# Performance work log

Measured on AMD Instinct MI355X. Metric: run time of the kernel, lower is better.

Reference implementation:

```python
import jax, jax.numpy as jnp
import numpy as np

B, L, D, H = 2, 2048, 1024, 16


def setup_inputs() -> dict:
    key = jax.random.key(0)
    ks = jax.random.split(key, 6)
    return {
        "x": jax.random.normal(ks[0], (B, L, D), dtype=jnp.float32),
        "w_qkv": jax.random.normal(ks[1], (3 * D, D), dtype=jnp.float32) * (D ** -0.5),
        "b_qkv": jax.random.normal(ks[2], (3 * D,), dtype=jnp.float32) * 0.02,
        "w_out": jax.random.normal(ks[3], (D, D), dtype=jnp.float32) * (D ** -0.5),
        "b_out": jax.random.normal(ks[4], (D,), dtype=jnp.float32) * 0.02,
        "lam": jnp.float32(0.5),
        "heads": H,
    }


def reference(x, w_qkv, b_qkv, w_out, b_out, lam, heads):
    b, l, d = x.shape
    dh = d // heads
    scale = d ** -0.5  # NOTE: module scales by d_model**-0.5, not head_dim**-0.5

    qkv = x @ w_qkv.T + b_qkv                      # [B, L, 3D]
    qkv = qkv.reshape(b, l, 3, heads, dh)
    qkv = jnp.transpose(qkv, (2, 0, 3, 1, 4))      # [3, B, H, L, dh]
    q, k, v = qkv[0], qkv[1], qkv[2]

    k_prev = jnp.roll(k, shift=1, axis=2)          # roll along sequence dim

    s_cur = jnp.einsum("bhqd,bhkd->bhqk", q, k) * scale
    s_prev = jnp.einsum("bhqd,bhkd->bhqk", q, k_prev) * scale

    a1 = jax.nn.softmax(s_cur, axis=-1)
    a2 = jax.nn.softmax(s_prev, axis=-1)
    diff = lam * (a1 - a2)                         # dropout = identity (eval)

    o = jnp.einsum("bhqk,bhkd->bhqd", diff, v)     # [B, H, L, dh]
    o = jnp.transpose(o, (0, 2, 1, 3)).reshape(b, l, d)
    return o @ w_out.T + b_out
```

## Files before the change

kernel.cpp:

```cpp
#include <hip/hip_runtime.h>
#include <hip/hip_bf16.h>
#include <stdint.h>


typedef __attribute__((ext_vector_type(8))) short s16x8;
typedef __attribute__((ext_vector_type(4))) short s16x4;
typedef __attribute__((ext_vector_type(4))) float f32x4;
typedef __attribute__((ext_vector_type(4))) unsigned int u32x4;

__device__ __forceinline__ float bf2f(unsigned short u) {
    union { unsigned int i; float f; } x; x.i = ((unsigned int)u) << 16; return x.f;
}
__device__ __forceinline__ unsigned short f2bf(float f) {
    union { float f; unsigned int i; } x; x.f = f;
    unsigned int r = x.i + 0x7FFFu + ((x.i >> 16) & 1u);
    return (unsigned short)(r >> 16);
}

__device__ __forceinline__ unsigned int cvtpk(float lo, float hi) {
    unsigned int r;
    asm("v_cvt_pk_bf16_f32 %0, %1, %2" : "=v"(r) : "v"(lo), "v"(hi));
    return r;
}

__device__ __forceinline__ void gload16(const void* g, void* l) {
    auto gp = reinterpret_cast<const __attribute__((address_space(1))) unsigned int*>(
        reinterpret_cast<uintptr_t>(g));
    auto lp = reinterpret_cast<__attribute__((address_space(3))) unsigned int*>(
        reinterpret_cast<uintptr_t>(l));
    __builtin_amdgcn_global_load_lds(gp, lp, 16, 0, 0);
}

__global__ __launch_bounds__(256) void cvt_all(
    const float* __restrict__ x, const float* __restrict__ wq,
    const float* __restrict__ wo,
    unsigned short* __restrict__ xb, unsigned short* __restrict__ wqb,
    unsigned short* __restrict__ wob)
{
    int i4 = blockIdx.x * 256 + threadIdx.x;
    const float* src; unsigned short* dst; int off;
    if (i4 < 1048576)            { src = x;  dst = xb;  off = i4; }
    else if (i4 < 1048576 + 786432) { src = wq; dst = wqb; off = i4 - 1048576; }
    else                         { src = wo; dst = wob; off = i4 - 1835008; }
    float4 v = ((const float4*)src)[off];
    ushort4 u;
    u.x = f2bf(v.x); u.y = f2bf(v.y); u.z = f2bf(v.z); u.w = f2bf(v.w);
    ((ushort4*)dst)[off] = u;
}

__global__ __launch_bounds__(256) void vd_transpose(
    const unsigned short* __restrict__ qkvb, unsigned short* __restrict__ vdt)
{
    __shared__ unsigned short T[64][72];
    const int tid = threadIdx.x;
    const int j0 = blockIdx.x * 64;
    const int bh = blockIdx.y, b = bh >> 4, h = bh & 15;
    const unsigned short* vb = qkvb + (size_t)b * 2048 * 3072 + 2048 + h * 64;

    int r = tid >> 2, cq = tid & 3;
    int rp = (r & 35) | ((r & 12) << 1) | ((r & 16) >> 2);
    int j = j0 + r, jn = (j + 1) & 2047;
    const unsigned short* p0 = vb + (size_t)j  * 3072 + cq * 16;
    const unsigned short* p1 = vb + (size_t)jn * 3072 + cq * 16;
    s16x8 a0 = *(const s16x8*)p0, a1 = *(const s16x8*)(p0 + 8);
    s16x8 b0 = *(const s16x8*)p1, b1 = *(const s16x8*)(p1 + 8);
#pragma unroll
    for (int u = 0; u < 8; ++u)
        T[cq * 16 + u][rp] = f2bf(bf2f((unsigned short)a0[u]) - bf2f((unsigned short)b0[u]));
#pragma unroll
    for (int u = 0; u < 8; ++u)
        T[cq * 16 + 8 + u][rp] = f2bf(bf2f((unsigned short)a1[u]) - bf2f((unsigned short)b1[u]));
    __syncthreads();

    int row = tid >> 2, sc = tid & 3;
    s16x8 o0 = *(const s16x8*)&T[row][sc * 16];
    s16x8 o1 = *(const s16x8*)&T[row][sc * 16 + 8];
    unsigned short* dst = vdt + ((size_t)bh * 64 + row) * 2048 + j0 + sc * 16;
    *(s16x8*)dst = o0;
    *(s16x8*)(dst + 8) = o1;
}

template <int OUT_BF16, int BN>
__global__ __launch_bounds__(256) void gemm_nt_mfma(
    const unsigned short* __restrict__ A,
    const unsigned short* __restrict__ Bm,
    const float* __restrict__ bias,
    void* __restrict__ C,
    int M, int N, int K, int nscale, float smul)
{
    constexpr int NT = BN / 32;
    __shared__ unsigned short As[2][128][32];
    __shared__ unsigned short Bs[2][BN][32];

    const int tid = threadIdx.x;
    const int wave = tid >> 6, lane = tid & 63;
    const int quad = lane >> 4, ln = lane & 15;
    const int wm = (wave >> 1) * 64, wn = (wave & 1) * (NT * 16);
    const int m0 = blockIdx.y * 128, n0 = blockIdx.x * BN;
    const int rA = wave * 16 + (lane >> 2);
    const int gsl = lane & 3;

    f32x4 acc[4][NT];
#pragma unroll
    for (int mt = 0; mt < 4; ++mt)
#pragma unroll
        for (int nt = 0; nt < NT; ++nt) acc[mt][nt] = f32x4{0.f, 0.f, 0.f, 0.f};

    auto stage = [&](int p, int k0) {
#pragma unroll
        for (int q = 0; q < 2; ++q) {
            int row = q * 64 + rA;
            int kg = gsl ^ ((row >> 1) & 3);
            gload16(A + (size_t)(m0 + row) * K + k0 + kg * 8,
                    &As[p][q * 64 + wave * 16][0]);
            if (q * 64 < BN)
                gload16(Bm + (size_t)(n0 + row) * K + k0 + kg * 8,
                        &Bs[p][q * 64 + wave * 16][0]);
        }
    };

    stage(0, 0);
    __syncthreads();
    int p = 0;
    for (int k0 = 0; k0 < K; k0 += 32) {
        if (k0 + 32 < K) stage(p ^ 1, k0 + 32);
        s16x8 af[4], bfr[NT];
#pragma unroll
        for (int mt = 0; mt < 4; ++mt) {
            int rr = wm + mt * 16 + ln;
            af[mt] = *(const s16x8*)&As[p][rr][((quad ^ ((rr >> 1) & 3)) & 3) * 8];
        }
#pragma unroll
        for (int nt = 0; nt < NT; ++nt) {
            int rr = wn + nt * 16 + ln;
            bfr[nt] = *(const s16x8*)&Bs[p][rr][((quad ^ ((rr >> 1) & 3)) & 3) * 8];
        }
#pragma unroll
        for (int mt = 0; mt < 4; ++mt)
#pragma unroll
            for (int nt = 0; nt < NT; ++nt)
                acc[mt][nt] = __builtin_amdgcn_mfma_f32_16x16x32_bf16(
                    af[mt], bfr[nt], acc[mt][nt], 0, 0, 0);
        __syncthreads();
        p ^= 1;
    }

    float bb[NT];
#pragma unroll
    for (int nt = 0; nt < NT; ++nt) bb[nt] = bias[n0 + wn + nt * 16 + ln];
#pragma unroll
    for (int mt = 0; mt < 4; ++mt)
#pragma unroll
        for (int nt = 0; nt < NT; ++nt) {
            int col = n0 + wn + nt * 16 + ln;
            float sc = (col < nscale) ? smul : 1.f;
#pragma unroll
            for (int rg = 0; rg < 4; ++rg) {
                int row = m0 + wm + mt * 16 + quad * 4 + rg;
                float v = (acc[mt][nt][rg] + bb[nt]) * sc;
                if (OUT_BF16)
                    ((unsigned short*)C)[(size_t)row * N + col] = f2bf(v);
                else
                    ((float*)C)[(size_t)row * N + col] = v;
            }
        }
}

__global__ __launch_bounds__(512) void diff_attn_v10(
    const unsigned short* __restrict__ qkv,
    const unsigned short* __restrict__ vdt,
    const float* __restrict__ lam_p,
    unsigned short* __restrict__ o_ws)
{
    constexpr int L = 2048, TD = 3072;

    __shared__ __align__(16) unsigned char smem[65536];
    auto Ks = reinterpret_cast<unsigned short(*)[64][64]>(smem);
    auto Vs = reinterpret_cast<unsigned short(*)[64][64]>(smem + 32768);
    auto Red = reinterpret_cast<f32x4(*)[2][4][64]>(smem);
    auto Lred = reinterpret_cast<float(*)[2][64]>(smem + 32768);

    const int tid = threadIdx.x;
    const int wave = tid >> 6, lane = tid & 63;
    const int qw = wave & 3, jw = wave >> 2;
    const int quad = lane >> 4, ln = lane & 15;
    const int bh = blockIdx.y, b = bh >> 4, h = bh & 15;
    const int q0 = blockIdx.x * 128;
    const size_t seqbase = (size_t)b * L;
    const unsigned short* base = qkv + seqbase * TD + h * 64;
    const unsigned short* kb = base + 1024;
    const unsigned short* vbase = vdt + (size_t)bh * 64 * 2048;

    const int lsl = lane >> 3;
    const int cgl = (lane & 7) ^ lsl;

    const float lam = lam_p[0];
    asm volatile("" :: "v"(lam));

    s16x8 qf[2][2];
#pragma unroll
    for (int s = 0; s < 2; ++s) {
        const unsigned short* qrow =
            base + (size_t)(q0 + qw * 32 + s * 16 + ln) * TD;
        qf[s][0] = *(const s16x8*)(qrow + quad * 8);
        qf[s][1] = *(const s16x8*)(qrow + 32 + quad * 8);
    }

    const unsigned short* kstage = kb + (size_t)(wave * 8 + lsl) * TD + cgl * 8;
    const unsigned short* vstage = vbase + (size_t)(wave * 8 + lsl) * 2048 + cgl * 8;

    f32x4 Ot[2][4];
    f32x4 lacc[2];
#pragma unroll
    for (int s = 0; s < 2; ++s) {
        lacc[s] = f32x4{0.f, 0.f, 0.f, 0.f};
#pragma unroll
        for (int mt = 0; mt < 4; ++mt) Ot[s][mt] = f32x4{0.f, 0.f, 0.f, 0.f};
    }

    const s16x8 ones8 = {(short)0x3F80, (short)0x3F80, (short)0x3F80, (short)0x3F80,
                         (short)0x3F80, (short)0x3F80, (short)0x3F80, (short)0x3F80};
    const int kx0 = (quad ^ (ln & 7)) << 3;
    const int kx1 = ((quad + 4) ^ (ln & 7)) << 3;
    const int vx  = (((jw * 4 + quad) ^ (ln & 7))) << 3;

    auto body = [&](auto cc, auto ccs, int j0s) {
        constexpr int c  = decltype(cc)::value;
        constexpr int cs = decltype(ccs)::value;

        gload16(kstage + (size_t)j0s * TD, &Ks[cs][wave * 8][0]);
        gload16(vstage + j0s,              &Vs[cs][wave * 8][0]);

        f32x4 ST[2][2];
        __builtin_amdgcn_s_setprio(1);
#pragma unroll
        for (int t = 0; t < 2; ++t) {
            const int t2 = jw * 2 + t;
            s16x8 k0 = *(const s16x8*)&Ks[c][t2 * 16 + ln][kx0];
            s16x8 k1 = *(const s16x8*)&Ks[c][t2 * 16 + ln][kx1];
#pragma unroll
            for (int s = 0; s < 2; ++s) {
                f32x4 z = f32x4{0.f, 0.f, 0.f, 0.f};
                z = __builtin_amdgcn_mfma_f32_16x16x32_bf16(k0, qf[s][0], z, 0, 0, 0);
                z = __builtin_amdgcn_mfma_f32_16x16x32_bf16(k1, qf[s][1], z, 0, 0, 0);
                ST[s][t] = z;
            }
        }
        __builtin_amdgcn_s_setprio(0);

        s16x8 pf8[2];
#pragma unroll
        for (int s = 0; s < 2; ++s) {
            unsigned int w[4];
#pragma unroll
            for (int t = 0; t < 2; ++t) {
                float e0 = __builtin_amdgcn_exp2f(ST[s][t][0]);
                float e1 = __builtin_amdgcn_exp2f(ST[s][t][1]);
                float e2 = __builtin_amdgcn_exp2f(ST[s][t][2]);
                float e3 = __builtin_amdgcn_exp2f(ST[s][t][3]);
                w[t * 2]     = cvtpk(e0, e1);
                w[t * 2 + 1] = cvtpk(e2, e3);
            }
            pf8[s] = __builtin_bit_cast(s16x8, (u32x4){w[0], w[1], w[2], w[3]});
        }

        __builtin_amdgcn_s_setprio(1);
#pragma unroll
        for (int s = 0; s < 2; ++s)
            lacc[s] = __builtin_amdgcn_mfma_f32_16x16x32_bf16(
                ones8, pf8[s], lacc[s], 0, 0, 0);
#pragma unroll
        for (int mt = 0; mt < 4; ++mt) {
            s16x8 vf = *(const s16x8*)&Vs[c][mt * 16 + ln][vx];
#pragma unroll
            for (int s = 0; s < 2; ++s)
                Ot[s][mt] = __builtin_amdgcn_mfma_f32_16x16x32_bf16(
                    vf, pf8[s], Ot[s][mt], 0, 0, 0);
        }
        __builtin_amdgcn_s_setprio(0);

        asm volatile("s_waitcnt vmcnt(2)" ::: "memory");
        __builtin_amdgcn_s_barrier();
        asm volatile("" ::: "memory");
    };

    gload16(kstage, &Ks[0][wave * 8][0]);
    gload16(vstage, &Vs[0][wave * 8][0]);
    gload16(kstage + (size_t)64 * TD, &Ks[1][wave * 8][0]);
    gload16(vstage + 64,              &Vs[1][wave * 8][0]);
    asm volatile("s_waitcnt vmcnt(2)" ::: "memory");
    __builtin_amdgcn_s_barrier();
    asm volatile("" ::: "memory");

    using I0 = std::integral_constant<int, 0>;
    using I1 = std::integral_constant<int, 1>;
    using I2 = std::integral_constant<int, 2>;
    using I3 = std::integral_constant<int, 3>;
    for (int it = 0; it < 8; ++it) {
        const int kt4 = it * 4;
        body(I0{}, I2{}, ((kt4 + 2) & 31) * 64);
        body(I1{}, I3{}, ((kt4 + 3) & 31) * 64);
        body(I2{}, I0{}, ((kt4 + 4) & 31) * 64);
        body(I3{}, I1{}, ((kt4 + 5) & 31) * 64);
    }

    __syncthreads();

    if (jw == 1) {
#pragma unroll
        for (int s = 0; s < 2; ++s) {
            Lred[qw][s][lane] = lacc[s][0];
#pragma unroll
            for (int mt = 0; mt < 4; ++mt) Red[qw][s][mt][lane] = Ot[s][mt];
        }
    }
    __syncthreads();
    if (jw == 0) {
#pragma unroll
        for (int s = 0; s < 2; ++s) {
            float lsum = lacc[s][0] + Lred[qw][s][lane];
            float inv = lam / lsum;
            int row = q0 + qw * 32 + s * 16 + ln;
            unsigned short* orow = o_ws + (seqbase + row) * 1024 + h * 64 + quad * 4;
#pragma unroll
            for (int mt = 0; mt < 4; ++mt) {
                f32x4 r = Red[qw][s][mt][lane];
                ushort4 u;
                u.x = f2bf((Ot[s][mt][0] + r[0]) * inv);
                u.y = f2bf((Ot[s][mt][1] + r[1]) * inv);
                u.z = f2bf((Ot[s][mt][2] + r[2]) * inv);
                u.w = f2bf((Ot[s][mt][3] + r[3]) * inv);
                *(ushort4*)(orow + mt * 16) = u;
            }
        }
    }
}

extern "C" void kernel_launch(void* const* d_in, const int* in_sizes, int n_in,
                              void* d_out, int out_size, void* d_ws, size_t ws_size,
                              hipStream_t stream) {
    const float* x     = (const float*)d_in[0];
    const float* w_qkv = (const float*)d_in[1];
    const float* b_qkv = (const float*)d_in[2];
    const float* w_out = (const float*)d_in[3];
    const float* b_out = (const float*)d_in[4];
    const float* lam   = (const float*)d_in[5];
    float* out = (float*)d_out;

    unsigned short* xb   = (unsigned short*)d_ws;
    unsigned short* wqb  = xb   + (size_t)4096 * 1024;
    unsigned short* wob  = wqb  + (size_t)3072 * 1024;
    unsigned short* qkvb = wob  + (size_t)1024 * 1024;
    unsigned short* ob   = qkvb + (size_t)4096 * 3072;
    unsigned short* vdt  = ob   + (size_t)4096 * 1024;

    cvt_all<<<8192, 256, 0, stream>>>(x, w_qkv, w_out, xb, wqb, wob);

    gemm_nt_mfma<1, 128><<<dim3(24, 32), 256, 0, stream>>>(
        xb, wqb, b_qkv, qkvb, 4096, 3072, 1024, 1024, 0.045084222f);

    vd_transpose<<<dim3(32, 32), 256, 0, stream>>>(qkvb, vdt);

    diff_attn_v10<<<dim3(16, 32), 512, 0, stream>>>(qkvb, vdt, lam, ob);

    gemm_nt_mfma<0, 64><<<dim3(16, 32), 256, 0, stream>>>(
        ob, wob, b_out, out, 4096, 1024, 1024, 0, 1.f);
}
```

Measured before the change: 184.5 us.

## Fuse fp32-to-bf16 conversion into GEMM tile staging, drop separate convert kernel

Removes the standalone conversion kernel that turned x, w_qkv and w_out into bf16 copies. The GEMMs now load fp32 tiles into registers, pack them to bf16 and write them into LDS after the MFMA step, which keeps prefetch overlap. This saves a launch and the bf16 write and re-read round trip. In exchange the GEMMs read twice as many bytes from global memory, and the weights are re-converted by every block that touches them instead of once.

```diff
diff --git a/kernel.cpp b/kernel.cpp
--- a/kernel.cpp
+++ b/kernel.cpp
@@ -29,23 +29,6 @@
     auto lp = reinterpret_cast<__attribute__((address_space(3))) unsigned int*>(
         reinterpret_cast<uintptr_t>(l));
     __builtin_amdgcn_global_load_lds(gp, lp, 16, 0, 0);
-}
-
-__global__ __launch_bounds__(256) void cvt_all(
-    const float* __restrict__ x, const float* __restrict__ wq,
-    const float* __restrict__ wo,
-    unsigned short* __restrict__ xb, unsigned short* __restrict__ wqb,
-    unsigned short* __restrict__ wob)
-{
-    int i4 = blockIdx.x * 256 + threadIdx.x;
-    const float* src; unsigned short* dst; int off;
-    if (i4 < 1048576)            { src = x;  dst = xb;  off = i4; }
-    else if (i4 < 1048576 + 786432) { src = wq; dst = wqb; off = i4 - 1048576; }
-    else                         { src = wo; dst = wob; off = i4 - 1835008; }
-    float4 v = ((const float4*)src)[off];
-    ushort4 u;
-    u.x = f2bf(v.x); u.y = f2bf(v.y); u.z = f2bf(v.z); u.w = f2bf(v.w);
-    ((ushort4*)dst)[off] = u;
 }
 
 __global__ __launch_bounds__(256) void vd_transpose(
@@ -80,10 +63,10 @@
     *(s16x8*)(dst + 8) = o1;
 }
 
-template <int OUT_BF16, int BN>
+template <int OUT_BF16, int BN, int CVT_A, int CVT_B>
 __global__ __launch_bounds__(256) void gemm_nt_mfma(
-    const unsigned short* __restrict__ A,
-    const unsigned short* __restrict__ Bm,
+    const void* __restrict__ Ap,
+    const void* __restrict__ Bp,
     const float* __restrict__ bias,
     void* __restrict__ C,
     int M, int N, int K, int nscale, float smul)
@@ -106,24 +89,61 @@
 #pragma unroll
         for (int nt = 0; nt < NT; ++nt) acc[mt][nt] = f32x4{0.f, 0.f, 0.f, 0.f};
 
-    auto stage = [&](int p, int k0) {
+    float4 ra[2][2], rb[2][2];
+
+    auto ld8f = [&](const float* src, int row, int k0, float4* d) {
+        int kg = gsl ^ ((row >> 1) & 3);
+        const float* p = src + (size_t)row * K + k0 + kg * 8;
+        d[0] = *(const float4*)p;
+        d[1] = *(const float4*)(p + 4);
+    };
+
+    auto stage_loads = [&](int pn, int k0) {
 #pragma unroll
         for (int q = 0; q < 2; ++q) {
             int row = q * 64 + rA;
-            int kg = gsl ^ ((row >> 1) & 3);
-            gload16(A + (size_t)(m0 + row) * K + k0 + kg * 8,
-                    &As[p][q * 64 + wave * 16][0]);
-            if (q * 64 < BN)
-                gload16(Bm + (size_t)(n0 + row) * K + k0 + kg * 8,
-                        &Bs[p][q * 64 + wave * 16][0]);
-        }
-    };
-
-    stage(0, 0);
+            if (CVT_A) {
+                ld8f((const float*)Ap, m0 + row, k0, ra[q]);
+            } else {
+                int kg = gsl ^ ((row >> 1) & 3);
+                gload16((const unsigned short*)Ap + (size_t)(m0 + row) * K + k0 + kg * 8,
+                        &As[pn][q * 64 + wave * 16][0]);
+            }
+            if (q * 64 < BN) {
+                if (CVT_B) {
+                    ld8f((const float*)Bp, n0 + row, k0, rb[q]);
+                } else {
+                    int kg = gsl ^ ((row >> 1) & 3);
+                    gload16((const unsigned short*)Bp + (size_t)(n0 + row) * K + k0 + kg * 8,
+                            &Bs[pn][q * 64 + wave * 16][0]);
+                }
+            }
+        }
+    };
+
+    auto wr16 = [&](unsigned short* dstbase, const float4* v) {
+        u32x4 w = { cvtpk(v[0].x, v[0].y), cvtpk(v[0].z, v[0].w),
+                    cvtpk(v[1].x, v[1].y), cvtpk(v[1].z, v[1].w) };
+        *(u32x4*)(dstbase + lane * 8) = w;
+    };
+
+    auto stage_writes = [&](int pn) {
+#pragma unroll
+        for (int q = 0; q < 2; ++q) {
+            if (CVT_A) wr16(&As[pn][q * 64 + wave * 16][0], ra[q]);
+            if (CVT_B && q * 64 < BN) wr16(&Bs[pn][q * 64 + wave * 16][0], rb[q]);
+        }
+    };
+
+    stage_loads(0, 0);
+    stage_writes(0);
     __syncthreads();
+
     int p = 0;
     for (int k0 = 0; k0 < K; k0 += 32) {
-        if (k0 + 32 < K) stage(p ^ 1, k0 + 32);
+        const bool more = (k0 + 32 < K);
+        if (more) stage_loads(p ^ 1, k0 + 32);
+
         s16x8 af[4], bfr[NT];
 #pragma unroll
         for (int mt = 0; mt < 4; ++mt) {
@@ -141,6 +161,8 @@
             for (int nt = 0; nt < NT; ++nt)
                 acc[mt][nt] = __builtin_amdgcn_mfma_f32_16x16x32_bf16(
                     af[mt], bfr[nt], acc[mt][nt], 0, 0, 0);
+
+        if (more) stage_writes(p ^ 1);
         __syncthreads();
         p ^= 1;
     }
@@ -354,15 +376,13 @@
     unsigned short* ob   = qkvb + (size_t)4096 * 3072;
     unsigned short* vdt  = ob   + (size_t)4096 * 1024;
 
-    cvt_all<<<8192, 256, 0, stream>>>(x, w_qkv, w_out, xb, wqb, wob);
-
-    gemm_nt_mfma<1, 128><<<dim3(24, 32), 256, 0, stream>>>(
-        xb, wqb, b_qkv, qkvb, 4096, 3072, 1024, 1024, 0.045084222f);
+    gemm_nt_mfma<1, 128, 1, 1><<<dim3(24, 32), 256, 0, stream>>>(
+        x, w_qkv, b_qkv, qkvb, 4096, 3072, 1024, 1024, 0.045084222f);
 
     vd_transpose<<<dim3(32, 32), 256, 0, stream>>>(qkvb, vdt);
 
     diff_attn_v10<<<dim3(16, 32), 512, 0, stream>>>(qkvb, vdt, lam, ob);
 
-    gemm_nt_mfma<0, 64><<<dim3(16, 32), 256, 0, stream>>>(
-        ob, wob, b_out, out, 4096, 1024, 1024, 0, 1.f);
-}
+    gemm_nt_mfma<0, 64, 0, 1><<<dim3(16, 32), 256, 0, stream>>>(
+        ob, w_out, b_out, out, 4096, 1024, 1024, 0, 1.f);
+}
```

New measurement: 188.0 us. About the same (+1.9%).
